# Optimization experiments

Measured on AMD Instinct MI355X. Metric: run time of the kernel, lower is better.

The kernel has to match this reference:

```python
import jax, jax.numpy as jnp
import numpy as np

HID = 1024
HEADS = 16
HEAD_DIM = HID // HEADS


def setup_inputs() -> dict:
    key = jax.random.key(0)
    ks = jax.random.split(key, 6)
    N, S = 4, 4096
    scale = 1.0 / np.sqrt(HID)
    return {
        "x": jax.random.normal(ks[0], (N, S, HID), dtype=jnp.float32),
        "Wq": jax.random.normal(ks[1], (HID, HID), dtype=jnp.float32) * scale,
        "Wk": jax.random.normal(ks[2], (HID, HID), dtype=jnp.float32) * scale,
        "Wv": jax.random.normal(ks[3], (HID, HID), dtype=jnp.float32) * scale,
        "Wo": jax.random.normal(ks[4], (HID, HID), dtype=jnp.float32) * scale,
        "bo": jnp.zeros((HID,), dtype=jnp.float32),
    }


def reference(x, Wq, Wk, Wv, Wo, bo):
    N, S, _ = x.shape
    # Linear projections (torch Linear: y = x @ W^T; here W stored as [in, out])
    q = (x @ Wq).reshape(N, S, HEADS, HEAD_DIM)
    k = (x @ Wk).reshape(N, S, HEADS, HEAD_DIM)
    v = (x @ Wv).reshape(N, S, HEADS, HEAD_DIM)
    # transpose(1,2): [N, H, S, D]
    q = jnp.swapaxes(q, 1, 2)
    k = jnp.swapaxes(k, 1, 2)
    v = jnp.swapaxes(v, 1, 2)
    # Faithful to source: einsum labels 'nqhd,nkhd->nqk' applied to [N,H,S,D]
    # tensors => contracts over (seq, head_dim); energy is [N, H, H].
    energy = jnp.einsum('nahd,nbhd->nab', q, k)  # a,b index heads; h indexes seq
    attention = jax.nn.softmax(energy / np.sqrt(HEAD_DIM), axis=2)  # [N, H, H]
    # 'nqk,nkhd->nqhd' on [N,H,H] x [N,H,S,D] -> [N,H,S,D]
    out = jnp.einsum('nab,nbsd->nasd', attention, v)
    # Faithful reshape (mixes head/seq axes exactly as torch .reshape does)
    out = out.reshape(N, S, HID)
    return out @ Wo + bo
```

## Files before the change

### kernel.cpp

```cpp
#include <hip/hip_runtime.h>
#include <hip/hip_bf16.h>

#define HID 1024
#define SEQ 4096
#define NBATCH 4

typedef __attribute__((ext_vector_type(8))) short bf16x8;
typedef __attribute__((ext_vector_type(4))) float f32x4;

__device__ __forceinline__ unsigned short f2bf(float f) {
  union { float f; unsigned u; } v; v.f = f;
  unsigned r = v.u + 0x7fffu + ((v.u >> 16) & 1u);
  return (unsigned short)(r >> 16);
}
__device__ __forceinline__ float bf2f(unsigned short h) {
  union { unsigned u; float f; } v; v.u = ((unsigned)h) << 16; return v.f;
}
__device__ __forceinline__ void gload16(const void* g, void* l) {
  __builtin_amdgcn_global_load_lds(
      (const __attribute__((address_space(1))) unsigned*)g,
      (__attribute__((address_space(3))) unsigned*)l, 16, 0, 0);
}

__global__ __launch_bounds__(256) void split_x_kernel(
    const float* __restrict__ x, unsigned short* __restrict__ xhi,
    unsigned short* __restrict__ xthi, unsigned short* __restrict__ xtlo) {
  const int n = blockIdx.z;
  const int c0 = blockIdx.x * 32;
  const int s0 = blockIdx.y * 32;
  __shared__ float t[32][33];
  const int tx = threadIdx.x & 31, ty = threadIdx.x >> 5;
  const float* xp = x + (size_t)n * SEQ * HID;
#pragma unroll
  for (int i = 0; i < 32; i += 8) {
    const float f = xp[(size_t)(s0 + ty + i) * HID + c0 + tx];
    t[ty + i][tx] = f;
    xhi[(size_t)n * SEQ * HID + (size_t)(s0 + ty + i) * HID + c0 + tx] = f2bf(f);
  }
  __syncthreads();
#pragma unroll
  for (int i = 0; i < 32; i += 8) {
    const float f = t[tx][ty + i];
    const size_t di = (size_t)n * HID * SEQ + (size_t)(c0 + ty + i) * SEQ + s0 + tx;
    const unsigned short hb = f2bf(f);
    xthi[di] = hb;
    xtlo[di] = f2bf(f - bf2f(hb));
  }
}

__global__ __launch_bounds__(256) void split_w_kernel(
    const float* __restrict__ Wq, const float* __restrict__ Wv,
    const float* __restrict__ Wo, unsigned short* qh, unsigned short* ql,
    unsigned short* vh, unsigned short* oh) {
  const float* W; unsigned short* dh; unsigned short* dl;
  if (blockIdx.z == 0)      { W = Wq; dh = qh; dl = ql; }
  else if (blockIdx.z == 1) { W = Wv; dh = vh; dl = nullptr; }
  else                      { W = Wo; dh = oh; dl = nullptr; }
  __shared__ float t[32][33];
  const int tx = threadIdx.x & 31, ty = threadIdx.x >> 5;
  const int c0 = blockIdx.x * 32, r0 = blockIdx.y * 32;
#pragma unroll
  for (int i = 0; i < 32; i += 8)
    t[ty + i][tx] = W[(size_t)(r0 + ty + i) * HID + c0 + tx];
  __syncthreads();
#pragma unroll
  for (int i = 0; i < 32; i += 8) {
    const float f = t[tx][ty + i];
    const size_t di = (size_t)(c0 + ty + i) * HID + (r0 + tx);
    const unsigned short hb = f2bf(f);
    dh[di] = hb;
    if (dl) dl[di] = f2bf(f - bf2f(hb));
  }
}

template <bool SPLIT3, bool OUT_BF16, bool BIAS>
__global__ __launch_bounds__(256, 2) void gemm_kernel(
    const unsigned short* __restrict__ A1, const unsigned short* __restrict__ A2,
    const unsigned short* __restrict__ B1, const unsigned short* __restrict__ B2,
    float* __restrict__ Cf, unsigned short* __restrict__ Cb,
    const float* __restrict__ bias, int M, int N, int Kd) {
  constexpr int TILE = 128 * 32;
  constexpr int NT = SPLIT3 ? 4 : 2;
  __shared__ unsigned short lds[NT * TILE];
  unsigned short* As1 = lds;
  unsigned short* Bs1 = lds + TILE;
  unsigned short* As2 = SPLIT3 ? lds + 2 * TILE : nullptr;
  unsigned short* Bs2 = SPLIT3 ? lds + 3 * TILE : nullptr;

  const int tid = threadIdx.x;
  const int lane = tid & 63;
  const int w = tid >> 6;
  const int wr = w >> 1, wc = w & 1;
  const int m0 = blockIdx.x * 128, n0 = blockIdx.y * 128;
  const int z = blockIdx.z;

  const unsigned short* pA1 = A1 + (size_t)z * M * Kd;
  const unsigned short* pA2 = SPLIT3 ? A2 + (size_t)z * M * Kd : nullptr;

  f32x4 acc[4][4] = {};

  const int fr = lane & 15;
  const int k8 = (lane >> 4) * 8;

  for (int kt = 0; kt < Kd; kt += 32) {
#pragma unroll
    for (int i = 0; i < 2; ++i) {
      const int ob = i * 4096 + tid * 16;
      const int r = ob >> 6;
      const int ce = (ob & 63) >> 1;
      gload16(pA1 + (size_t)(m0 + r) * Kd + kt + ce, (char*)As1 + ob);
      gload16(B1 + (size_t)(n0 + r) * Kd + kt + ce, (char*)Bs1 + ob);
      if (SPLIT3) {
        gload16(pA2 + (size_t)(m0 + r) * Kd + kt + ce, (char*)As2 + ob);
        gload16(B2 + (size_t)(n0 + r) * Kd + kt + ce, (char*)Bs2 + ob);
      }
    }
    __syncthreads();
    bf16x8 a1[4], b1[4], a2[4], b2[4];
#pragma unroll
    for (int m = 0; m < 4; ++m) {
      const int row = wr * 64 + m * 16 + fr;
      a1[m] = *(const bf16x8*)&As1[row * 32 + k8];
      if (SPLIT3) a2[m] = *(const bf16x8*)&As2[row * 32 + k8];
    }
#pragma unroll
    for (int n = 0; n < 4; ++n) {
      const int row = wc * 64 + n * 16 + fr;
      b1[n] = *(const bf16x8*)&Bs1[row * 32 + k8];
      if (SPLIT3) b2[n] = *(const bf16x8*)&Bs2[row * 32 + k8];
    }
#pragma unroll
    for (int m = 0; m < 4; ++m)
#pragma unroll
      for (int n = 0; n < 4; ++n) {
        acc[m][n] = __builtin_amdgcn_mfma_f32_16x16x32_bf16(a1[m], b1[n], acc[m][n], 0, 0, 0);
        if (SPLIT3) {
          acc[m][n] = __builtin_amdgcn_mfma_f32_16x16x32_bf16(a1[m], b2[n], acc[m][n], 0, 0, 0);
          acc[m][n] = __builtin_amdgcn_mfma_f32_16x16x32_bf16(a2[m], b1[n], acc[m][n], 0, 0, 0);
        }
      }
    __syncthreads();
  }

  const int r4 = (lane >> 4) * 4;
#pragma unroll
  for (int m = 0; m < 4; ++m) {
    const int row0 = m0 + wr * 64 + m * 16 + r4;
#pragma unroll
    for (int n = 0; n < 4; ++n) {
      const int col = n0 + wc * 64 + n * 16 + fr;
      const float bv = BIAS ? bias[col] : 0.0f;
#pragma unroll
      for (int r2 = 0; r2 < 4; ++r2) {
        const size_t idx = (size_t)z * M * N + (size_t)(row0 + r2) * N + col;
        const float vv = acc[m][n][r2] + bv;
        if (OUT_BF16) Cb[idx] = f2bf(vv);
        else Cf[idx] = vv;
      }
    }
  }
}

__global__ __launch_bounds__(256, 2) void gram_kernel(
    const unsigned short* __restrict__ Xthi, const unsigned short* __restrict__ Xtlo,
    float* __restrict__ Gpart) {
  constexpr int TILE = 128 * 32;
  __shared__ unsigned short lds[4 * TILE];
  unsigned short* As1 = lds;
  unsigned short* Bs1 = lds + TILE;
  unsigned short* As2 = lds + 2 * TILE;
  unsigned short* Bs2 = lds + 3 * TILE;

  const int tid = threadIdx.x;
  const int lane = tid & 63;
  const int w = tid >> 6;
  const int wr = w >> 1, wc = w & 1;
  const int m0 = blockIdx.x * 128, n0 = blockIdx.y * 128;
  const int nb = blockIdx.z >> 1, chunk = blockIdx.z & 1;

  const size_t abase = (size_t)nb * HID * SEQ + (size_t)chunk * 2048;
  const unsigned short* pH = Xthi + abase;
  const unsigned short* pL = Xtlo + abase;

  f32x4 acc[4][4] = {};
  const int fr = lane & 15;
  const int k8 = (lane >> 4) * 8;

  for (int kt = 0; kt < 2048; kt += 32) {
#pragma unroll
    for (int i = 0; i < 2; ++i) {
      const int ob = i * 4096 + tid * 16;
      const int r = ob >> 6;
      const int ce = (ob & 63) >> 1;
      gload16(pH + (size_t)(m0 + r) * SEQ + kt + ce, (char*)As1 + ob);
      gload16(pH + (size_t)(n0 + r) * SEQ + kt + ce, (char*)Bs1 + ob);
      gload16(pL + (size_t)(m0 + r) * SEQ + kt + ce, (char*)As2 + ob);
      gload16(pL + (size_t)(n0 + r) * SEQ + kt + ce, (char*)Bs2 + ob);
    }
    __syncthreads();
    bf16x8 a1[4], b1[4], a2[4], b2[4];
#pragma unroll
    for (int m = 0; m < 4; ++m) {
      const int row = wr * 64 + m * 16 + fr;
      a1[m] = *(const bf16x8*)&As1[row * 32 + k8];
      a2[m] = *(const bf16x8*)&As2[row * 32 + k8];
    }
#pragma unroll
    for (int n = 0; n < 4; ++n) {
      const int row = wc * 64 + n * 16 + fr;
      b1[n] = *(const bf16x8*)&Bs1[row * 32 + k8];
      b2[n] = *(const bf16x8*)&Bs2[row * 32 + k8];
    }
#pragma unroll
    for (int m = 0; m < 4; ++m)
#pragma unroll
      for (int n = 0; n < 4; ++n) {
        acc[m][n] = __builtin_amdgcn_mfma_f32_16x16x32_bf16(a1[m], b1[n], acc[m][n], 0, 0, 0);
        acc[m][n] = __builtin_amdgcn_mfma_f32_16x16x32_bf16(a1[m], b2[n], acc[m][n], 0, 0, 0);
        acc[m][n] = __builtin_amdgcn_mfma_f32_16x16x32_bf16(a2[m], b1[n], acc[m][n], 0, 0, 0);
      }
    __syncthreads();
  }

  float* Cf = Gpart + ((size_t)chunk * NBATCH + nb) * HID * HID;
  const int r4 = (lane >> 4) * 4;
#pragma unroll
  for (int m = 0; m < 4; ++m) {
    const int row0 = m0 + wr * 64 + m * 16 + r4;
#pragma unroll
    for (int n = 0; n < 4; ++n) {
      const int col = n0 + wc * 64 + n * 16 + fr;
#pragma unroll
      for (int r2 = 0; r2 < 4; ++r2)
        Cf[(size_t)(row0 + r2) * HID + col] = acc[m][n][r2];
    }
  }
}

__global__ __launch_bounds__(256) void reduce_split_kernel(
    const float* __restrict__ Gp, unsigned short* __restrict__ ghi,
    unsigned short* __restrict__ glo) {
  const size_t i = ((size_t)blockIdx.x * 256 + threadIdx.x) * 4;
  const float4 a = *(const float4*)(Gp + i);
  const float4 b = *(const float4*)(Gp + i + (size_t)NBATCH * HID * HID);
  const float f[4] = {a.x + b.x, a.y + b.y, a.z + b.z, a.w + b.w};
  ushort4 h, l;
  unsigned short hh[4], ll[4];
#pragma unroll
  for (int j = 0; j < 4; ++j) {
    hh[j] = f2bf(f[j]);
    ll[j] = f2bf(f[j] - bf2f(hh[j]));
  }
  h.x = hh[0]; h.y = hh[1]; h.z = hh[2]; h.w = hh[3];
  l.x = ll[0]; l.y = ll[1]; l.z = ll[2]; l.w = ll[3];
  *(ushort4*)(ghi + i) = h;
  *(ushort4*)(glo + i) = l;
}

__global__ __launch_bounds__(256) void energy_kernel(
    const float* __restrict__ Q, const float* __restrict__ Kq,
    float* __restrict__ energy, size_t qstride, size_t kstride) {
  const int n = blockIdx.y;
  const int s0 = blockIdx.x * 32;
  __shared__ float qs[16 * 68];
  __shared__ float ks[16 * 68];
  const int tid = threadIdx.x;
  const int a = tid >> 4, b = tid & 15;
  const int hb = (tid * 4) >> 6, d0 = (tid * 4) & 63;
  const float* Qn = Q + (size_t)n * qstride;
  const float* Kn = Kq + (size_t)n * kstride;
  float acc = 0.0f;
  for (int s = s0; s < s0 + 32; ++s) {
    __syncthreads();
    const float4 q4 = ((const float4*)(Qn + (size_t)s * HID))[tid];
    const float4 k4 = ((const float4*)(Kn + (size_t)s * HID))[tid];
    float* qp = qs + hb * 68 + d0;
    qp[0] = q4.x; qp[1] = q4.y; qp[2] = q4.z; qp[3] = q4.w;
    float* kp = ks + hb * 68 + d0;
    kp[0] = k4.x; kp[1] = k4.y; kp[2] = k4.z; kp[3] = k4.w;
    __syncthreads();
    float dot = 0.0f;
#pragma unroll
    for (int d = 0; d < 64; ++d) dot += qs[a * 68 + d] * ks[b * 68 + d];
    acc += dot;
  }
  atomicAdd(&energy[n * 256 + a * 16 + b], acc);
}

__global__ void softmax_kernel(const float* __restrict__ energy,
                               float* __restrict__ att) {
  const int t = threadIdx.x;
  const float* e = energy + t * 16;
  float m = -3.0e38f;
#pragma unroll
  for (int b = 0; b < 16; ++b) m = fmaxf(m, e[b]);
  float p[16];
  float ssum = 0.0f;
#pragma unroll
  for (int b = 0; b < 16; ++b) { p[b] = expf((e[b] - m) * 0.125f); ssum += p[b]; }
  const float inv = 1.0f / ssum;
#pragma unroll
  for (int b = 0; b < 16; ++b) att[t * 16 + b] = p[b] * inv;
}

__global__ __launch_bounds__(256) void out2_kernel(
    const unsigned short* __restrict__ V, const float* __restrict__ att,
    unsigned short* __restrict__ out2) {
  const int n = blockIdx.y, sg = blockIdx.x;
  __shared__ unsigned short vl[16 * 1032];
  __shared__ float al[256];
  const int tid = threadIdx.x;
  al[tid] = att[n * 256 + tid];
  const unsigned short* Vbp = V + ((size_t)n * SEQ + (size_t)sg * 16) * HID;
#pragma unroll
  for (int j = 0; j < 16; ++j) {
    const ushort4 u = *(const ushort4*)(Vbp + (size_t)j * HID + tid * 4);
    *(ushort4*)&vl[j * 1032 + tid * 4] = u;
  }
  __syncthreads();
  const int c0 = tid * 4;
  const int rr = c0 >> 6, d = c0 & 63;
  float vb[16][4];
#pragma unroll
  for (int b = 0; b < 16; ++b)
#pragma unroll
    for (int j = 0; j < 4; ++j)
      vb[b][j] = bf2f(vl[rr * 1032 + b * 64 + d + j]);
#pragma unroll
  for (int h = 0; h < 16; ++h) {
    float o0 = 0, o1 = 0, o2 = 0, o3 = 0;
#pragma unroll
    for (int b = 0; b < 16; ++b) {
      const float wgt = al[h * 16 + b];
      o0 += wgt * vb[b][0]; o1 += wgt * vb[b][1];
      o2 += wgt * vb[b][2]; o3 += wgt * vb[b][3];
    }
    ushort4 u;
    u.x = f2bf(o0); u.y = f2bf(o1); u.z = f2bf(o2); u.w = f2bf(o3);
    *(ushort4*)(out2 + ((size_t)n * SEQ + (size_t)(h * 256 + sg)) * HID + c0) = u;
  }
}

extern "C" void kernel_launch(void* const* d_in, const int* in_sizes, int n_in,
                              void* d_out, int out_size, void* d_ws, size_t ws_size,
                              hipStream_t stream) {
  (void)in_sizes; (void)n_in; (void)out_size; (void)ws_size;
  const float* x  = (const float*)d_in[0];
  const float* Wq = (const float*)d_in[1];
  const float* Wk = (const float*)d_in[2];
  const float* Wv = (const float*)d_in[3];
  const float* Wo = (const float*)d_in[4];
  const float* bo = (const float*)d_in[5];
  float* out = (float*)d_out;

  char* ws = (char*)d_ws;
  size_t off = 0;
  auto alloc = [&](size_t bytes) {
    char* p = ws + off;
    off += (bytes + 255) & ~(size_t)255;
    return p;
  };
  const size_t XE = (size_t)NBATCH * SEQ * HID;
  const size_t GE = (size_t)NBATCH * HID * HID;
  unsigned short* Xhi  = (unsigned short*)alloc(XE * 2);
  unsigned short* Xthi = (unsigned short*)alloc(XE * 2);
  unsigned short* Xtlo = (unsigned short*)alloc(XE * 2);
  unsigned short* WqhT = (unsigned short*)alloc((size_t)HID * HID * 2);
  unsigned short* WqlT = (unsigned short*)alloc((size_t)HID * HID * 2);
  unsigned short* WvhT = (unsigned short*)alloc((size_t)HID * HID * 2);
  unsigned short* WohT = (unsigned short*)alloc((size_t)HID * HID * 2);
  float* Gpart = (float*)alloc(2 * GE * 4);
  unsigned short* Ghi = (unsigned short*)alloc(GE * 2);
  unsigned short* Glo = (unsigned short*)alloc(GE * 2);
  float* energy = (float*)alloc((size_t)NBATCH * 256 * 4);
  float* att    = (float*)alloc((size_t)NBATCH * 256 * 4);
  unsigned short* Vb = Xthi;
  float* M1 = Gpart;
  unsigned short* O2 = Xtlo;

  split_x_kernel<<<dim3(HID / 32, SEQ / 32, NBATCH), 256, 0, stream>>>(
      x, Xhi, Xthi, Xtlo);
  split_w_kernel<<<dim3(HID / 32, HID / 32, 3), 256, 0, stream>>>(
      Wq, Wv, Wo, WqhT, WqlT, WvhT, WohT);

  gram_kernel<<<dim3(HID / 128, HID / 128, NBATCH * 2), 256, 0, stream>>>(
      Xthi, Xtlo, Gpart);
  reduce_split_kernel<<<(unsigned)(GE / 4 / 256), 256, 0, stream>>>(
      Gpart, Ghi, Glo);

  gemm_kernel<false, true, false><<<dim3(SEQ / 128, HID / 128, NBATCH), 256, 0, stream>>>(
      Xhi, nullptr, WvhT, nullptr, nullptr, Vb, nullptr, SEQ, HID, HID);

  gemm_kernel<true, false, false><<<dim3(HID / 128, HID / 128, NBATCH), 256, 0, stream>>>(
      Ghi, Glo, WqhT, WqlT, M1, nullptr, nullptr, HID, HID, HID);

  hipMemsetAsync(energy, 0, (size_t)NBATCH * 256 * 4, stream);
  energy_kernel<<<dim3(HID / 32, NBATCH), 256, 0, stream>>>(
      M1, Wk, energy, (size_t)HID * HID, 0);
  softmax_kernel<<<1, 64, 0, stream>>>(energy, att);
  out2_kernel<<<dim3(256, NBATCH), 256, 0, stream>>>(Vb, att, O2);

  gemm_kernel<false, false, true><<<dim3(SEQ / 128, HID / 128, NBATCH), 256, 0, stream>>>(
      O2, nullptr, WohT, nullptr, out, nullptr, bo, SEQ, HID, HID);
}
```

Before: 439.9 us.

## Exploit Gram matrix symmetry with triangular tiles, three-way K split, vectorized transpose

The Gram kernel now computes only lower-triangular 128x128 tiles (36 instead of 64 per batch) and splits the K dimension three ways to keep the grid filled. The reduce kernel sums the three partials and fills the upper triangle by transposing mirrored tiles through shared memory. The x split/transpose kernel moves to 64x64 tiles with float4 loads and 16-byte stores. This roughly halves Gram MFMA work at the cost of an extra partial buffer and a more complex reduce.

```diff
diff --git a/kernel.cpp b/kernel.cpp
--- a/kernel.cpp
+++ b/kernel.cpp
@@ -7,6 +7,7 @@
 
 typedef __attribute__((ext_vector_type(8))) short bf16x8;
 typedef __attribute__((ext_vector_type(4))) float f32x4;
+typedef __attribute__((ext_vector_type(8))) unsigned short u16x8;
 
 __device__ __forceinline__ unsigned short f2bf(float f) {
   union { float f; unsigned u; } v; v.f = f;
@@ -26,26 +27,39 @@
     const float* __restrict__ x, unsigned short* __restrict__ xhi,
     unsigned short* __restrict__ xthi, unsigned short* __restrict__ xtlo) {
   const int n = blockIdx.z;
-  const int c0 = blockIdx.x * 32;
-  const int s0 = blockIdx.y * 32;
-  __shared__ float t[32][33];
-  const int tx = threadIdx.x & 31, ty = threadIdx.x >> 5;
+  const int c0 = blockIdx.x * 64;
+  const int s0 = blockIdx.y * 64;
+  __shared__ float t[64][65];
+  const int tid = threadIdx.x;
+  const int rr = tid >> 4;
+  const int cc = (tid & 15) * 4;
   const float* xp = x + (size_t)n * SEQ * HID;
-#pragma unroll
-  for (int i = 0; i < 32; i += 8) {
-    const float f = xp[(size_t)(s0 + ty + i) * HID + c0 + tx];
-    t[ty + i][tx] = f;
-    xhi[(size_t)n * SEQ * HID + (size_t)(s0 + ty + i) * HID + c0 + tx] = f2bf(f);
+  unsigned short* xhp = xhi + (size_t)n * SEQ * HID;
+#pragma unroll
+  for (int p = 0; p < 4; ++p) {
+    const int row = rr + p * 16;
+    const float4 v = *(const float4*)(xp + (size_t)(s0 + row) * HID + c0 + cc);
+    t[row][cc] = v.x; t[row][cc + 1] = v.y; t[row][cc + 2] = v.z; t[row][cc + 3] = v.w;
+    ushort4 h;
+    h.x = f2bf(v.x); h.y = f2bf(v.y); h.z = f2bf(v.z); h.w = f2bf(v.w);
+    *(ushort4*)(xhp + (size_t)(s0 + row) * HID + c0 + cc) = h;
   }
   __syncthreads();
-#pragma unroll
-  for (int i = 0; i < 32; i += 8) {
-    const float f = t[tx][ty + i];
-    const size_t di = (size_t)n * HID * SEQ + (size_t)(c0 + ty + i) * SEQ + s0 + tx;
-    const unsigned short hb = f2bf(f);
-    xthi[di] = hb;
-    xtlo[di] = f2bf(f - bf2f(hb));
-  }
+  const int c = tid >> 2;
+  const int sb = (tid & 3) * 16;
+  const size_t tbase = (size_t)n * HID * SEQ + (size_t)(c0 + c) * SEQ + s0 + sb;
+  unsigned short hbuf[16] __attribute__((aligned(16)));
+  unsigned short lbuf[16] __attribute__((aligned(16)));
+#pragma unroll
+  for (int k = 0; k < 16; ++k) {
+    const float f = t[sb + k][c];
+    hbuf[k] = f2bf(f);
+    lbuf[k] = f2bf(f - bf2f(hbuf[k]));
+  }
+  *(u16x8*)(xthi + tbase) = *(const u16x8*)&hbuf[0];
+  *(u16x8*)(xthi + tbase + 8) = *(const u16x8*)&hbuf[8];
+  *(u16x8*)(xtlo + tbase) = *(const u16x8*)&lbuf[0];
+  *(u16x8*)(xtlo + tbase + 8) = *(const u16x8*)&lbuf[8];
 }
 
 __global__ __launch_bounds__(256) void split_w_kernel(
@@ -98,7 +112,6 @@
   const unsigned short* pA2 = SPLIT3 ? A2 + (size_t)z * M * Kd : nullptr;
 
   f32x4 acc[4][4] = {};
-
   const int fr = lane & 15;
   const int k8 = (lane >> 4) * 8;
 
@@ -175,10 +188,19 @@
   const int lane = tid & 63;
   const int w = tid >> 6;
   const int wr = w >> 1, wc = w & 1;
-  const int m0 = blockIdx.x * 128, n0 = blockIdx.y * 128;
-  const int nb = blockIdx.z >> 1, chunk = blockIdx.z & 1;
-
-  const size_t abase = (size_t)nb * HID * SEQ + (size_t)chunk * 2048;
+
+  int rb = 0;
+  {
+    const int t = blockIdx.x;
+    while ((rb + 1) * (rb + 2) / 2 <= t) ++rb;
+  }
+  const int cb = blockIdx.x - rb * (rb + 1) / 2;
+  const int m0 = rb * 128, n0 = cb * 128;
+  const int nb = blockIdx.z / 3, chunk = blockIdx.z % 3;
+  const int kbeg = (chunk == 0) ? 0 : (chunk == 1 ? 1376 : 2752);
+  const int kend = (chunk == 0) ? 1376 : (chunk == 1 ? 2752 : 4096);
+
+  const size_t abase = (size_t)nb * HID * SEQ;
   const unsigned short* pH = Xthi + abase;
   const unsigned short* pL = Xtlo + abase;
 
@@ -186,7 +208,7 @@
   const int fr = lane & 15;
   const int k8 = (lane >> 4) * 8;
 
-  for (int kt = 0; kt < 2048; kt += 32) {
+  for (int kt = kbeg; kt < kend; kt += 32) {
 #pragma unroll
     for (int i = 0; i < 2; ++i) {
       const int ob = i * 4096 + tid * 16;
@@ -240,21 +262,72 @@
 __global__ __launch_bounds__(256) void reduce_split_kernel(
     const float* __restrict__ Gp, unsigned short* __restrict__ ghi,
     unsigned short* __restrict__ glo) {
-  const size_t i = ((size_t)blockIdx.x * 256 + threadIdx.x) * 4;
-  const float4 a = *(const float4*)(Gp + i);
-  const float4 b = *(const float4*)(Gp + i + (size_t)NBATCH * HID * HID);
-  const float f[4] = {a.x + b.x, a.y + b.y, a.z + b.z, a.w + b.w};
-  ushort4 h, l;
-  unsigned short hh[4], ll[4];
-#pragma unroll
-  for (int j = 0; j < 4; ++j) {
-    hh[j] = f2bf(f[j]);
-    ll[j] = f2bf(f[j] - bf2f(hh[j]));
-  }
-  h.x = hh[0]; h.y = hh[1]; h.z = hh[2]; h.w = hh[3];
-  l.x = ll[0]; l.y = ll[1]; l.z = ll[2]; l.w = ll[3];
-  *(ushort4*)(ghi + i) = h;
-  *(ushort4*)(glo + i) = l;
+  const int nb = blockIdx.z;
+  const int rt = blockIdx.y, ct = blockIdx.x;
+  const size_t HH = (size_t)HID * HID;
+  const float* g0 = Gp + (size_t)nb * HH;
+  const float* g1 = g0 + (size_t)NBATCH * HH;
+  const float* g2 = g1 + (size_t)NBATCH * HH;
+  unsigned short* oh = ghi + (size_t)nb * HH;
+  unsigned short* ol = glo + (size_t)nb * HH;
+  const int tid = threadIdx.x;
+  const int rr = tid >> 4, cc = (tid & 15) * 4;
+  const bool mirrored = (rt >> 1) < (ct >> 1);
+  __shared__ float t[64][65];
+
+  if (!mirrored) {
+#pragma unroll
+    for (int p = 0; p < 4; ++p) {
+      const size_t idx = (size_t)(rt * 64 + rr + p * 16) * HID + ct * 64 + cc;
+      const float4 a = *(const float4*)(g0 + idx);
+      const float4 b = *(const float4*)(g1 + idx);
+      const float4 cv = *(const float4*)(g2 + idx);
+      const float f[4] = {a.x + b.x + cv.x, a.y + b.y + cv.y,
+                          a.z + b.z + cv.z, a.w + b.w + cv.w};
+      ushort4 h, l;
+      unsigned short hh[4], ll[4];
+#pragma unroll
+      for (int j = 0; j < 4; ++j) {
+        hh[j] = f2bf(f[j]);
+        ll[j] = f2bf(f[j] - bf2f(hh[j]));
+      }
+      h.x = hh[0]; h.y = hh[1]; h.z = hh[2]; h.w = hh[3];
+      l.x = ll[0]; l.y = ll[1]; l.z = ll[2]; l.w = ll[3];
+      *(ushort4*)(oh + idx) = h;
+      *(ushort4*)(ol + idx) = l;
+    }
+  } else {
+#pragma unroll
+    for (int p = 0; p < 4; ++p) {
+      const int lr = rr + p * 16;
+      const size_t idx = (size_t)(ct * 64 + lr) * HID + rt * 64 + cc;
+      const float4 a = *(const float4*)(g0 + idx);
+      const float4 b = *(const float4*)(g1 + idx);
+      const float4 cv = *(const float4*)(g2 + idx);
+      t[lr][cc]     = a.x + b.x + cv.x;
+      t[lr][cc + 1] = a.y + b.y + cv.y;
+      t[lr][cc + 2] = a.z + b.z + cv.z;
+      t[lr][cc + 3] = a.w + b.w + cv.w;
+    }
+    __syncthreads();
+#pragma unroll
+    for (int p = 0; p < 4; ++p) {
+      const int orow = rr + p * 16;
+      const size_t idx = (size_t)(rt * 64 + orow) * HID + ct * 64 + cc;
+      ushort4 h, l;
+      unsigned short hh[4], ll[4];
+#pragma unroll
+      for (int j = 0; j < 4; ++j) {
+        const float f = t[cc + j][orow];
+        hh[j] = f2bf(f);
+        ll[j] = f2bf(f - bf2f(hh[j]));
+      }
+      h.x = hh[0]; h.y = hh[1]; h.z = hh[2]; h.w = hh[3];
+      l.x = ll[0]; l.y = ll[1]; l.z = ll[2]; l.w = ll[3];
+      *(ushort4*)(oh + idx) = h;
+      *(ushort4*)(ol + idx) = l;
+    }
+  }
 }
 
 __global__ __launch_bounds__(256) void energy_kernel(
@@ -369,7 +442,7 @@
   unsigned short* WqlT = (unsigned short*)alloc((size_t)HID * HID * 2);
   unsigned short* WvhT = (unsigned short*)alloc((size_t)HID * HID * 2);
   unsigned short* WohT = (unsigned short*)alloc((size_t)HID * HID * 2);
-  float* Gpart = (float*)alloc(2 * GE * 4);
+  float* Gpart = (float*)alloc(3 * GE * 4);
   unsigned short* Ghi = (unsigned short*)alloc(GE * 2);
   unsigned short* Glo = (unsigned short*)alloc(GE * 2);
   float* energy = (float*)alloc((size_t)NBATCH * 256 * 4);
@@ -378,15 +451,13 @@
   float* M1 = Gpart;
   unsigned short* O2 = Xtlo;
 
-  split_x_kernel<<<dim3(HID / 32, SEQ / 32, NBATCH), 256, 0, stream>>>(
+  split_x_kernel<<<dim3(HID / 64, SEQ / 64, NBATCH), 256, 0, stream>>>(
       x, Xhi, Xthi, Xtlo);
   split_w_kernel<<<dim3(HID / 32, HID / 32, 3), 256, 0, stream>>>(
       Wq, Wv, Wo, WqhT, WqlT, WvhT, WohT);
 
-  gram_kernel<<<dim3(HID / 128, HID / 128, NBATCH * 2), 256, 0, stream>>>(
-      Xthi, Xtlo, Gpart);
-  reduce_split_kernel<<<(unsigned)(GE / 4 / 256), 256, 0, stream>>>(
-      Gpart, Ghi, Glo);
+  gram_kernel<<<dim3(36, 1, NBATCH * 3), 256, 0, stream>>>(Xthi, Xtlo, Gpart);
+  reduce_split_kernel<<<dim3(16, 16, NBATCH), 256, 0, stream>>>(Gpart, Ghi, Glo);
 
   gemm_kernel<false, true, false><<<dim3(SEQ / 128, HID / 128, NBATCH), 256, 0, stream>>>(
       Xhi, nullptr, WvhT, nullptr, nullptr, Vb, nullptr, SEQ, HID, HID);
```

Result: faster. 427.8 us (-2.8%).
